# Kernel tuning notes

Measured on AMD Instinct MI355X. Metric: run time of the kernel, lower is better.

## Reference

```python
import jax, jax.numpy as jnp
import numpy as np

N = 40960      # nodes, level 0
E = 327680     # edges, level 0
N1 = 20480     # nodes after first graclus pool
E2 = 163840    # edges after first pool
N2 = 10240     # nodes after second graclus pool
B = 512        # graphs in batch
NCLS = 10


def seg_mean(v, idx, n):
    s = jax.ops.segment_sum(v, idx, num_segments=n)
    c = jax.ops.segment_sum(jnp.ones((idx.shape[0], 1), v.dtype), idx, num_segments=n)
    return s / jnp.maximum(c, 1.0)


def seg_max_f(v, idx, n):
    m = jax.ops.segment_max(v, idx, num_segments=n)
    return jnp.where(jnp.isneginf(m), 0.0, m)  # empty clusters -> 0


def cartesian(pos, ei):
    # PyG T.Cartesian(): cart = pos[row]-pos[col], normalized to [0,1]
    cart = pos[ei[0]] - pos[ei[1]]
    m = jnp.max(jnp.abs(cart))
    return cart / (2.0 * m) + 0.5


def nnconv_mean(x, ei, eattr, w1, b1, w2, b2, root, bias, n_nodes):
    # edge MLP -> per-edge weight matrix [E, Fin, Fout]
    fin, fout = root.shape
    h = jax.nn.relu(eattr @ w1 + b1) @ w2 + b2
    W = h.reshape(-1, fin, fout)
    src, dst = ei[0], ei[1]
    msg = jnp.einsum('ei,eio->eo', x[src], W)          # gather + per-edge matmul
    aggr = seg_mean(msg, dst, n_nodes)                 # scatter-mean
    return x @ root + aggr + bias


def setup_inputs() -> dict:
    key = jax.random.key(0)
    ks = jax.random.split(key, 24)
    inp = {}
    inp['x'] = jax.random.normal(ks[0], (N, 1), jnp.float32)
    inp['pos'] = jax.random.uniform(ks[1], (N, 2), jnp.float32) * 28.0
    inp['edge_attr'] = jax.random.uniform(ks[2], (E, 2), jnp.float32)
    inp['edge_index'] = jax.random.randint(ks[3], (2, E), 0, N)
    inp['batch'] = jnp.sort(jax.random.randint(ks[4], (N,), 0, B))
    inp['cluster1'] = jax.random.randint(ks[5], (N,), 0, N1)
    inp['edge_index2'] = jax.random.randint(ks[6], (2, E2), 0, N1)
    inp['cluster2'] = jax.random.randint(ks[7], (N1,), 0, N2)
    s = 0.1
    inp['nn1_w1'] = jax.random.normal(ks[8], (2, 25), jnp.float32) * s
    inp['nn1_b1'] = jnp.zeros((25,), jnp.float32)
    inp['nn1_w2'] = jax.random.normal(ks[9], (25, 32), jnp.float32) * s
    inp['nn1_b2'] = jnp.zeros((32,), jnp.float32)
    inp['root1'] = jax.random.normal(ks[10], (1, 32), jnp.float32) * s
    inp['bias1'] = jnp.zeros((32,), jnp.float32)
    inp['nn2_w1'] = jax.random.normal(ks[11], (2, 25), jnp.float32) * s
    inp['nn2_b1'] = jnp.zeros((25,), jnp.float32)
    inp['nn2_w2'] = jax.random.normal(ks[12], (25, 2048), jnp.float32) * s
    inp['nn2_b2'] = jnp.zeros((2048,), jnp.float32)
    inp['root2'] = jax.random.normal(ks[13], (32, 64), jnp.float32) * s
    inp['bias2'] = jnp.zeros((64,), jnp.float32)
    inp['fc1_w'] = jax.random.normal(ks[14], (64, 128), jnp.float32) * s
    inp['fc1_b'] = jnp.zeros((128,), jnp.float32)
    inp['fc2_w'] = jax.random.normal(ks[15], (128, NCLS), jnp.float32) * s
    inp['fc2_b'] = jnp.zeros((NCLS,), jnp.float32)
    return inp


def reference(x, pos, edge_attr, edge_index, batch, cluster1, edge_index2, cluster2,
              nn1_w1, nn1_b1, nn1_w2, nn1_b2, root1, bias1,
              nn2_w1, nn2_b1, nn2_w2, nn2_b2, root2, bias2,
              fc1_w, fc1_b, fc2_w, fc2_b):
    # conv1 + ELU
    x1 = jax.nn.elu(nnconv_mean(x, edge_index, edge_attr,
                                nn1_w1, nn1_b1, nn1_w2, nn1_b2, root1, bias1, N))
    # graclus max_pool (clusters precomputed): max features, mean pos, pooled batch
    x1p = seg_max_f(x1, cluster1, N1)
    pos1 = seg_mean(pos, cluster1, N1)
    batch1 = jnp.clip(jax.ops.segment_max(batch, cluster1, num_segments=N1), 0, B - 1)
    eattr2 = cartesian(pos1, edge_index2)  # transform=Cartesian on pooled graph
    # conv2 + ELU
    x2 = jax.nn.elu(nnconv_mean(x1p, edge_index2, eattr2,
                                nn2_w1, nn2_b1, nn2_w2, nn2_b2, root2, bias2, N1))
    # max_pool_x then global_mean_pool
    x2p = seg_max_f(x2, cluster2, N2)
    batch2 = jnp.clip(jax.ops.segment_max(batch1, cluster2, num_segments=N2), 0, B - 1)
    xg = seg_mean(x2p, batch2, B)
    h = jax.nn.elu(xg @ fc1_w + fc1_b)
    # dropout is identity in eval mode
    logits = h @ fc2_w + fc2_b
    return jax.nn.log_softmax(logits, axis=1)
```

## Files before the change

### kernel.cpp

```cpp
#include <hip/hip_runtime.h>
#include <hip/hip_bf16.h>
#include <limits.h>

#define NN   40960
#define EE   327680
#define NN1  20480
#define EE2  163840
#define NN2  10240
#define BB   512
#define NCLS 10

#define SEG1 160
#define SEG2 240
#define SEG3 320
#define SEG4 400
#define SBT  440

#define GEMM_BLKS 2080
#define R2_BLKS   640
#define CART_BLKS 640
#define PREP_BLKS 208

typedef short bf16x8 __attribute__((ext_vector_type(8)));
typedef float f32x4 __attribute__((ext_vector_type(4)));

__device__ __forceinline__ float elu_f(float v) { return v > 0.f ? v : (expf(v) - 1.f); }
__device__ __forceinline__ unsigned f2bf_bits(float v) {
    unsigned u = __float_as_uint(v);
    return (u + 0x7FFFu + ((u >> 16) & 1u)) >> 16;
}

__global__ void init_all(int* zbase, int zcount) {
    int i = blockIdx.x * 256 + threadIdx.x;
    if (i < zcount) zbase[i] = 0;
}

__global__ void deg_count(const int* __restrict__ ei, const int* __restrict__ ei2,
                          const int* __restrict__ cluster1, const int* __restrict__ cluster2,
                          int* deg1, int* degS, int* degD, int* degC1, int* degC2,
                          int* slot1, int* slotS, int* slotD, int* slotC1, int* slotC2) {
    int i = blockIdx.x * 256 + threadIdx.x;
    if (i < EE) slot1[i] = atomicAdd(deg1 + ei[EE + i], 1);
    if (i < EE2) {
        slotS[i] = atomicAdd(degS + ei2[i], 1);
        slotD[i] = atomicAdd(degD + ei2[EE2 + i], 1);
    }
    if (i < NN) slotC1[i] = atomicAdd(degC1 + cluster1[i], 1);
    if (i < NN1) slotC2[i] = atomicAdd(degC2 + cluster2[i], 1);
}

__global__ __launch_bounds__(256) void scan_partial(
    const int* __restrict__ deg1, const int* __restrict__ degS,
    const int* __restrict__ degD, const int* __restrict__ degC1,
    const int* __restrict__ degC2, int* __restrict__ part) {
    int b = blockIdx.x, t = threadIdx.x;
    const int* src;
    int off;
    if (b < SEG1)      { src = deg1;  off = b * 256; }
    else if (b < SEG2) { src = degS;  off = (b - SEG1) * 256; }
    else if (b < SEG3) { src = degD;  off = (b - SEG2) * 256; }
    else if (b < SEG4) { src = degC1; off = (b - SEG3) * 256; }
    else               { src = degC2; off = (b - SEG4) * 256; }
    int v = src[off + t];
#pragma unroll
    for (int o = 32; o; o >>= 1) v += __shfl_down(v, o, 64);
    __shared__ int sred[4];
    if ((t & 63) == 0) sred[t >> 6] = v;
    __syncthreads();
    if (t == 0) part[b] = sred[0] + sred[1] + sred[2] + sred[3];
}

__global__ __launch_bounds__(256) void scan_apply(
    const int* __restrict__ deg1, const int* __restrict__ degS,
    const int* __restrict__ degD, const int* __restrict__ degC1,
    const int* __restrict__ degC2, const int* __restrict__ part,
    int* rowptr1, int* rowptrS, int* rowptrD, int* rowptrC1, int* rowptrC2) {
    int b = blockIdx.x, t = threadIdx.x;
    const int* src;
    int* rp;
    int off, segLo;
    if (b < SEG1)      { src = deg1;  rp = rowptr1;  off = b * 256;          segLo = 0; }
    else if (b < SEG2) { src = degS;  rp = rowptrS;  off = (b - SEG1) * 256; segLo = SEG1; }
    else if (b < SEG3) { src = degD;  rp = rowptrD;  off = (b - SEG2) * 256; segLo = SEG2; }
    else if (b < SEG4) { src = degC1; rp = rowptrC1; off = (b - SEG3) * 256; segLo = SEG3; }
    else               { src = degC2; rp = rowptrC2; off = (b - SEG4) * 256; segLo = SEG4; }
    int bs = 0;
    for (int p = segLo + t; p < b; p += 256) bs += part[p];
#pragma unroll
    for (int o = 32; o; o >>= 1) bs += __shfl_down(bs, o, 64);
    __shared__ int sred[4];
    __shared__ int sh[256];
    if ((t & 63) == 0) sred[t >> 6] = bs;
    int v = src[off + t];
    sh[t] = v;
    __syncthreads();
    int base = sred[0] + sred[1] + sred[2] + sred[3];
#pragma unroll
    for (int o = 1; o < 256; o <<= 1) {
        int u = (t >= o) ? sh[t - o] : 0;
        __syncthreads();
        sh[t] += u;
        __syncthreads();
    }
    rp[off + t] = sh[t] - v + base;
    if (b == 0 && t == 0) {
        rowptr1[NN] = EE;
        rowptrS[NN1] = EE2;
        rowptrD[NN1] = EE2;
        rowptrC1[NN1] = NN;
        rowptrC2[NN2] = NN1;
    }
}

__global__ void fill_csr(const float* __restrict__ x, const float* __restrict__ ea,
                         const int* __restrict__ ei, const int* __restrict__ ei2,
                         const int* __restrict__ cluster1, const int* __restrict__ cluster2,
                         const int* __restrict__ rowptr1, const int* __restrict__ rowptrS,
                         const int* __restrict__ rowptrD, const int* __restrict__ rowptrC1,
                         const int* __restrict__ rowptrC2,
                         const int* __restrict__ slot1, const int* __restrict__ slotS,
                         const int* __restrict__ slotD, const int* __restrict__ slotC1,
                         const int* __restrict__ slotC2,
                         float4* __restrict__ eadj1, int4* __restrict__ cscRec,
                         int* __restrict__ memC1, int* __restrict__ memC2) {
    int i = blockIdx.x * 256 + threadIdx.x;
    if (i < EE) {
        int s = ei[i], d = ei[EE + i];
        eadj1[rowptr1[d] + slot1[i]] = make_float4(x[s], ea[2 * i], ea[2 * i + 1], 0.f);
    }
    if (i < EE2) {
        int s2 = ei2[i], d2 = ei2[EE2 + i];
        int q = rowptrS[s2] + slotS[i];
        int p2 = rowptrD[d2] + slotD[i];
        cscRec[q] = make_int4(s2, d2, p2, 0);
    }
    if (i < NN) memC1[rowptrC1[cluster1[i]] + slotC1[i]] = i;
    if (i < NN1) memC2[rowptrC2[cluster2[i]] + slotC2[i]] = i;
}

__global__ __launch_bounds__(256) void conv1_gather(
    const float* __restrict__ x, const int* __restrict__ rowptr1,
    const float4* __restrict__ eadj1,
    const float* __restrict__ w1, const float* __restrict__ b1,
    const float* __restrict__ w2, const float* __restrict__ b2,
    const float* __restrict__ root1, const float* __restrict__ bias1,
    float* __restrict__ x1) {
    int t = threadIdx.x;
    int j = t & 31;
    int n = blockIdx.x * 8 + (t >> 5);
    float w1x = 0.f, w1y = 0.f, b1j = 0.f;
    if (j < 25) { w1x = w1[j]; w1y = w1[25 + j]; b1j = b1[j]; }
    int r0 = rowptr1[n], r1 = rowptr1[n + 1];
    float agg = 0.f, sumx = 0.f;
    float4 e0 = make_float4(0.f, 0.f, 0.f, 0.f), e1 = e0;
    if (r0 < r1) e0 = eadj1[r0];
    if (r0 + 1 < r1) e1 = eadj1[r0 + 1];
    for (int p = r0; p < r1; p++) {
        float4 ed = e0;
        e0 = e1;
        if (p + 2 < r1) e1 = eadj1[p + 2];
        float h = fmaxf(fmaf(ed.y, w1x, fmaf(ed.z, w1y, b1j)), 0.f);
        agg = fmaf(ed.x, h, agg);
        sumx += ed.x;
    }
    float w2c[25];
#pragma unroll
    for (int k = 0; k < 25; k++) w2c[k] = w2[k * 32 + j];
    float m = sumx * b2[j];
#pragma unroll
    for (int k = 0; k < 25; k++) m = fmaf(__shfl(agg, k, 32), w2c[k], m);
    float deg = fmaxf((float)(r1 - r0), 1.f);
    float v = fmaf(x[n], root1[j], m / deg + bias1[j]);
    x1[(size_t)n * 32 + j] = elu_f(v);
}

__global__ __launch_bounds__(256) void pool1_gather(
    const float* __restrict__ x1, const float* __restrict__ pos,
    const int* __restrict__ batch, const int* __restrict__ rowptrC1,
    const int* __restrict__ memC1,
    float* __restrict__ x1p, unsigned short* __restrict__ x1pb,
    float* __restrict__ pos1, int* __restrict__ batch1) {
    int t = threadIdx.x;
    int j = t & 31;
    int c = blockIdx.x * 8 + (t >> 5);
    int r0 = rowptrC1[c], r1 = rowptrC1[c + 1];
    float mx = -INFINITY, sx = 0.f, sy = 0.f;
    int bmax = INT_MIN;
    for (int p = r0; p < r1; p++) {
        int v = memC1[p];
        mx = fmaxf(mx, x1[(size_t)v * 32 + j]);
        bmax = max(bmax, batch[v]);
        if (j == 0) {
            float2 pv = ((const float2*)pos)[v];
            sx += pv.x; sy += pv.y;
        }
    }
    float outv = (r0 < r1) ? mx : 0.f;
    x1p[(size_t)c * 32 + j] = outv;
    x1pb[(size_t)c * 32 + j] = (unsigned short)f2bf_bits(outv);
    if (j == 0) {
        float cn = fmaxf((float)(r1 - r0), 1.f);
        pos1[2 * c] = sx / cn;
        pos1[2 * c + 1] = sy / cn;
        batch1[c] = min(max(bmax, 0), BB - 1);
    }
}

__global__ void cartmax_prep(const float* __restrict__ pos1, const int* __restrict__ ei2,
                             unsigned* mBits,
                             const float* __restrict__ w2, const float* __restrict__ b2,
                             unsigned short* __restrict__ WextB) {
    int b = blockIdx.x;
    int t = threadIdx.x;
    if (b < CART_BLKS) {
        int e = b * 256 + t;
        float m = 0.f;
        if (e < EE2) {
            int r = ei2[e], c = ei2[EE2 + e];
            m = fmaxf(fabsf(pos1[2 * r] - pos1[2 * c]),
                      fabsf(pos1[2 * r + 1] - pos1[2 * c + 1]));
        }
        for (int off = 32; off; off >>= 1) m = fmaxf(m, __shfl_xor(m, off, 64));
        if ((t & 63) == 0) atomicMax(mBits, __float_as_uint(m));
    } else {
        int idx = (b - CART_BLKS) * 256 + t;
        if (idx >= 13 * 8 * 64 * 8) return;
        int j = idx & 7;
        int lane = (idx >> 3) & 63;
        int tile = (idx >> 9) & 7;
        int ky = idx >> 12;
        int h = tile >> 2, tt = tile & 3;
        int kmlp = 2 * ky + h;
        int o = tt * 16 + (lane & 15);
        int i = (lane >> 4) * 8 + j;
        float v = (kmlp < 25) ? w2[(size_t)kmlp * 2048 + i * 64 + o] : b2[i * 64 + o];
        WextB[idx] = (unsigned short)f2bf_bits(v);
    }
}

__global__ __launch_bounds__(256) void gemm_r2(
    const unsigned short* __restrict__ x1pb, const unsigned short* __restrict__ WextB,
    unsigned* __restrict__ Au,
    const int4* __restrict__ cscRec, const float* __restrict__ pos1,
    const float* __restrict__ w1, const float* __restrict__ b1,
    const unsigned* __restrict__ mBits, uint4* __restrict__ r2q) {
    int blk = blockIdx.x;
    int t = threadIdx.x;
    if (blk < GEMM_BLKS) {
        int lane = t & 63;
        int w = t >> 6;
        int bx = blk % 160;
        int ky = blk / 160;
        int m0 = bx * 128 + w * 32;
        int lo16 = lane & 15, hi4 = lane >> 4;
        bf16x8 bf[8];
        const bf16x8* Bp = (const bf16x8*)(WextB + (size_t)ky * 4096);
#pragma unroll
        for (int i = 0; i < 8; i++) bf[i] = Bp[i * 64 + lane];
        const f32x4 zero = {0.f, 0.f, 0.f, 0.f};
#pragma unroll
        for (int mt = 0; mt < 2; mt++) {
            int mbase = m0 + mt * 16;
            bf16x8 af = *(const bf16x8*)(x1pb + ((size_t)(mbase + lo16) * 32 + hi4 * 8));
            f32x4 acc[8];
#pragma unroll
            for (int i = 0; i < 8; i++)
                acc[i] = __builtin_amdgcn_mfma_f32_16x16x32_bf16(af, bf[i], zero, 0, 0, 0);
#pragma unroll
            for (int tt = 0; tt < 4; tt++) {
#pragma unroll
                for (int j = 0; j < 4; j++) {
                    int n = mbase + hi4 * 4 + j;
                    unsigned lo = f2bf_bits(acc[tt][j]);
                    unsigned hi = f2bf_bits(acc[4 + tt][j]);
                    Au[(size_t)n * 832 + ky * 64 + tt * 16 + lo16] = lo | (hi << 16);
                }
            }
        }
    } else {
        int q = (blk - GEMM_BLKS) * 256 + t;
        if (q >= EE2) return;
        int4 rec = cscRec[q];
        int s = rec.x, d = rec.y;
        float inv = 0.5f / __uint_as_float(*mBits);
        float2 ps = ((const float2*)pos1)[s];
        float2 pd = ((const float2*)pos1)[d];
        float cx = fmaf(ps.x - pd.x, inv, 0.5f);
        float cy = fmaf(ps.y - pd.y, inv, 0.5f);
        unsigned out[16];
#pragma unroll
        for (int ky = 0; ky < 13; ky++) {
            int k0 = 2 * ky, k1 = 2 * ky + 1;
            float rlo = fmaxf(fmaf(cx, w1[k0], fmaf(cy, w1[25 + k0], b1[k0])), 0.f);
            float rhi = 1.f;
            if (k1 < 25) rhi = fmaxf(fmaf(cx, w1[k1], fmaf(cy, w1[25 + k1], b1[k1])), 0.f);
            out[ky] = f2bf_bits(rlo) | (f2bf_bits(rhi) << 16);
        }
        out[13] = (unsigned)rec.z;
        out[14] = 0u; out[15] = 0u;
        uint4* dst = r2q + (size_t)q * 4;
        dst[0] = make_uint4(out[0], out[1], out[2], out[3]);
        dst[1] = make_uint4(out[4], out[5], out[6], out[7]);
        dst[2] = make_uint4(out[8], out[9], out[10], out[11]);
        dst[3] = make_uint4(out[12], out[13], out[14], out[15]);
    }
}

__global__ __launch_bounds__(256) void conv2_msg(
    const unsigned* __restrict__ Au, const uint4* __restrict__ r2q,
    const int* __restrict__ rowptrS, unsigned short* __restrict__ msgbuf) {
    int t = threadIdx.x;
    int lane = t & 63;
    int s = __builtin_amdgcn_readfirstlane(blockIdx.x * 4 + (t >> 6));
    unsigned au[13];
    const unsigned* Ab = Au + (size_t)s * 832 + lane;
#pragma unroll
    for (int ky = 0; ky < 13; ky++) au[ky] = Ab[ky * 64];
    int r0 = rowptrS[s], r1 = rowptrS[s + 1];
    uint4 A0, B0, C0, D0;
    if (r0 < r1) {
        const uint4* p4 = r2q + (size_t)r0 * 4;
        A0 = p4[0]; B0 = p4[1]; C0 = p4[2]; D0 = p4[3];
    }
    for (int q = r0; q < r1; q++) {
        uint4 a = A0, b = B0, c = C0, dd = D0;
        if (q + 1 < r1) {
            const uint4* p4 = r2q + (size_t)(q + 1) * 4;
            A0 = p4[0]; B0 = p4[1]; C0 = p4[2]; D0 = p4[3];
        }
        unsigned rr[13] = {a.x, a.y, a.z, a.w, b.x, b.y, b.z, b.w, c.x, c.y, c.z, c.w, dd.x};
        unsigned dstSlot = dd.y;
        float m0 = 0.f, m1 = 0.f;
#pragma unroll
        for (int ky = 0; ky < 13; ky++) {
            unsigned rp = rr[ky];
            unsigned ua = au[ky];
            m0 = fmaf(__uint_as_float(rp << 16), __uint_as_float(ua << 16), m0);
            m1 = fmaf(__uint_as_float(rp & 0xFFFF0000u), __uint_as_float(ua & 0xFFFF0000u), m1);
        }
        msgbuf[(size_t)dstSlot * 64 + lane] = (unsigned short)f2bf_bits(m0 + m1);
    }
}

__global__ __launch_bounds__(256) void conv2_fin(
    const unsigned short* __restrict__ msgbuf, const int* __restrict__ rowptrD,
    const float* __restrict__ x1p, const float* __restrict__ root2,
    const float* __restrict__ bias2, float* __restrict__ x2) {
    int t = threadIdx.x;
    int lane = t & 63;
    int n = blockIdx.x * 4 + (t >> 6);
    float Rr[32];
#pragma unroll
    for (int i = 0; i < 32; i++) Rr[i] = root2[i * 64 + lane];
    int r0 = rowptrD[n], r1 = rowptrD[n + 1];
    float acc = 0.f;
    for (int p = r0; p < r1; p++)
        acc += __uint_as_float((unsigned)msgbuf[(size_t)p * 64 + lane] << 16);
    float deg = fmaxf((float)(r1 - r0), 1.f);
    float xv = x1p[(size_t)n * 32 + (lane & 31)];
    float ra2 = bias2[lane];
#pragma unroll
    for (int i = 0; i < 32; i++) ra2 = fmaf(__shfl(xv, i, 64), Rr[i], ra2);
    x2[(size_t)n * 64 + lane] = elu_f(ra2 + acc / deg);
}

__global__ __launch_bounds__(256) void pool2_gather(
    const float* __restrict__ x2, const int* __restrict__ rowptrC2,
    const int* __restrict__ memC2, const int* __restrict__ batch1,
    float* __restrict__ xgsumS, float* __restrict__ gcntS) {
    int t = threadIdx.x;
    int lane = t & 63;
    int n2 = blockIdx.x * 4 + (t >> 6);
    int r0 = rowptrC2[n2], r1 = rowptrC2[n2 + 1];
    float mx = -INFINITY;
    int bmax = INT_MIN;
    for (int p = r0; p < r1; p++) {
        int m = memC2[p];
        mx = fmaxf(mx, x2[(size_t)m * 64 + lane]);
        bmax = max(bmax, batch1[m]);
    }
    float v = (r0 < r1) ? mx : 0.f;
    int b = min(max(bmax, 0), BB - 1);
    int shard = n2 & 7;
    atomicAdd(xgsumS + ((size_t)shard * BB + b) * 64 + lane, v);
    if (lane == 0) atomicAdd(gcntS + shard * BB + b, 1.f);
}

__global__ __launch_bounds__(128) void head_kernel(
    const float* __restrict__ xgsumS, const float* __restrict__ gcntS,
    const float* __restrict__ fc1w, const float* __restrict__ fc1b,
    const float* __restrict__ fc2w, const float* __restrict__ fc2b,
    float* __restrict__ out) {
    int b = blockIdx.x;
    int t = threadIdx.x;
    __shared__ float xg[64];
    __shared__ float h[128];
    __shared__ float lg[NCLS];
    __shared__ float red[2];
    __shared__ float cntsh;
    float s = 0.f;
    if (t < 64) {
#pragma unroll
        for (int sh = 0; sh < 8; sh++) s += xgsumS[((size_t)sh * BB + b) * 64 + t];
    }
    if (t == 64) {
        float c = 0.f;
#pragma unroll
        for (int sh = 0; sh < 8; sh++) c += gcntS[sh * BB + b];
        cntsh = fmaxf(c, 1.f);
    }
    __syncthreads();
    if (t < 64) xg[t] = s / cntsh;
    __syncthreads();
    float a1 = fc1b[t];
    for (int i = 0; i < 64; i++) a1 = fmaf(xg[i], fc1w[i * 128 + t], a1);
    h[t] = elu_f(a1);
    __syncthreads();
    if (t < NCLS) {
        float a = fc2b[t];
        for (int j = 0; j < 128; j++) a = fmaf(h[j], fc2w[j * NCLS + t], a);
        lg[t] = a;
    }
    __syncthreads();
    if (t == 0) {
        float mx = lg[0];
        for (int i = 1; i < NCLS; i++) mx = fmaxf(mx, lg[i]);
        float se = 0.f;
        for (int i = 0; i < NCLS; i++) se += expf(lg[i] - mx);
        red[0] = mx;
        red[1] = logf(se);
    }
    __syncthreads();
    if (t < NCLS) out[(size_t)b * NCLS + t] = lg[t] - red[0] - red[1];
}

extern "C" void kernel_launch(void* const* d_in, const int* in_sizes, int n_in,
                              void* d_out, int out_size, void* d_ws, size_t ws_size,
                              hipStream_t stream) {
    const float* x = (const float*)d_in[0];
    const float* pos = (const float*)d_in[1];
    const float* edge_attr = (const float*)d_in[2];
    const int* ei = (const int*)d_in[3];
    const int* batch = (const int*)d_in[4];
    const int* cluster1 = (const int*)d_in[5];
    const int* ei2 = (const int*)d_in[6];
    const int* cluster2 = (const int*)d_in[7];
    const float* nn1_w1 = (const float*)d_in[8];
    const float* nn1_b1 = (const float*)d_in[9];
    const float* nn1_w2 = (const float*)d_in[10];
    const float* nn1_b2 = (const float*)d_in[11];
    const float* root1 = (const float*)d_in[12];
    const float* bias1 = (const float*)d_in[13];
    const float* nn2_w1 = (const float*)d_in[14];
    const float* nn2_b1 = (const float*)d_in[15];
    const float* nn2_w2 = (const float*)d_in[16];
    const float* nn2_b2 = (const float*)d_in[17];
    const float* root2 = (const float*)d_in[18];
    const float* bias2 = (const float*)d_in[19];
    const float* fc1w = (const float*)d_in[20];
    const float* fc1b = (const float*)d_in[21];
    const float* fc2w = (const float*)d_in[22];
    const float* fc2b = (const float*)d_in[23];

    float* ws = (float*)d_ws;
    constexpr size_t OFF_DEG1 = 0;
    constexpr size_t OFF_DEGS = OFF_DEG1 + NN;
    constexpr size_t OFF_DEGD = OFF_DEGS + NN1;
    constexpr size_t OFF_DEGC1 = OFF_DEGD + NN1;
    constexpr size_t OFF_DEGC2 = OFF_DEGC1 + NN1;
    constexpr size_t OFF_XGS = OFF_DEGC2 + NN2;
    constexpr size_t OFF_GCS = OFF_XGS + (size_t)8 * BB * 64;
    constexpr size_t OFF_MBITS = OFF_GCS + 8 * BB;
    constexpr size_t ZTOT = OFF_MBITS + 4;
    constexpr size_t OFF_PART = ZTOT;
    constexpr size_t OFF_ROWPTR1 = OFF_PART + SBT;
    constexpr size_t OFF_ROWPTRS = OFF_ROWPTR1 + NN + 4;
    constexpr size_t OFF_ROWPTRD = OFF_ROWPTRS + NN1 + 4;
    constexpr size_t OFF_ROWPTRC1 = OFF_ROWPTRD + NN1 + 4;
    constexpr size_t OFF_ROWPTRC2 = OFF_ROWPTRC1 + NN1 + 4;
    constexpr size_t OFF_SLOT1 = OFF_ROWPTRC2 + NN2 + 4;
    constexpr size_t OFF_SLOTS = OFF_SLOT1 + EE;
    constexpr size_t OFF_SLOTD = OFF_SLOTS + EE2;
    constexpr size_t OFF_SLOTC1 = OFF_SLOTD + EE2;
    constexpr size_t OFF_SLOTC2 = OFF_SLOTC1 + NN;
    constexpr size_t OFF_CSCREC = OFF_SLOTC2 + NN1;
    constexpr size_t OFF_MEMC1 = OFF_CSCREC + (size_t)EE2 * 4;
    constexpr size_t OFF_MEMC2 = OFF_MEMC1 + NN;
    constexpr size_t OFF_X1 = OFF_MEMC2 + NN1;
    constexpr size_t OFF_X1P = OFF_X1 + (size_t)NN * 32;
    constexpr size_t OFF_X1PB = OFF_X1P + (size_t)NN1 * 32;
    constexpr size_t OFF_POS1 = OFF_X1PB + (size_t)NN1 * 16;
    constexpr size_t OFF_BATCH1 = OFF_POS1 + (size_t)NN1 * 2;
    constexpr size_t OFF_X2 = OFF_BATCH1 + NN1;
    constexpr size_t OFF_WEXTB = OFF_X2 + (size_t)NN1 * 64;
    constexpr size_t OFF_UA = OFF_WEXTB + 26624;
    constexpr size_t UASZ = (size_t)EE2 * 16;
    constexpr size_t OFF_MSG = OFF_UA + UASZ;
    constexpr size_t OFF_AU = OFF_MSG + (size_t)EE2 * 32;

    int* deg1 = (int*)(ws + OFF_DEG1);
    int* degS = (int*)(ws + OFF_DEGS);
    int* degD = (int*)(ws + OFF_DEGD);
    int* degC1 = (int*)(ws + OFF_DEGC1);
    int* degC2 = (int*)(ws + OFF_DEGC2);
    float* xgsumS = ws + OFF_XGS;
    float* gcntS = ws + OFF_GCS;
    unsigned* mBits = (unsigned*)(ws + OFF_MBITS);
    int* part = (int*)(ws + OFF_PART);
    int* rowptr1 = (int*)(ws + OFF_ROWPTR1);
    int* rowptrS = (int*)(ws + OFF_ROWPTRS);
    int* rowptrD = (int*)(ws + OFF_ROWPTRD);
    int* rowptrC1 = (int*)(ws + OFF_ROWPTRC1);
    int* rowptrC2 = (int*)(ws + OFF_ROWPTRC2);
    int* slot1 = (int*)(ws + OFF_SLOT1);
    int* slotS = (int*)(ws + OFF_SLOTS);
    int* slotD = (int*)(ws + OFF_SLOTD);
    int* slotC1 = (int*)(ws + OFF_SLOTC1);
    int* slotC2 = (int*)(ws + OFF_SLOTC2);
    int4* cscRec = (int4*)(ws + OFF_CSCREC);
    int* memC1 = (int*)(ws + OFF_MEMC1);
    int* memC2 = (int*)(ws + OFF_MEMC2);
    float* x1 = ws + OFF_X1;
    float* x1p = ws + OFF_X1P;
    unsigned short* x1pb = (unsigned short*)(ws + OFF_X1PB);
    float* pos1 = ws + OFF_POS1;
    int* batch1 = (int*)(ws + OFF_BATCH1);
    float* x2 = ws + OFF_X2;
    unsigned short* WextB = (unsigned short*)(ws + OFF_WEXTB);
    float4* eadj1 = (float4*)(ws + OFF_UA);
    uint4* r2q = (uint4*)(ws + OFF_UA);
    unsigned short* msgbuf = (unsigned short*)(ws + OFF_MSG);
    unsigned* Au = (unsigned*)(ws + OFF_AU);

    init_all<<<(int)((ZTOT + 255) / 256), 256, 0, stream>>>((int*)d_ws, (int)ZTOT);
    deg_count<<<EE / 256, 256, 0, stream>>>(ei, ei2, cluster1, cluster2,
                                            deg1, degS, degD, degC1, degC2,
                                            slot1, slotS, slotD, slotC1, slotC2);
    scan_partial<<<SBT, 256, 0, stream>>>(deg1, degS, degD, degC1, degC2, part);
    scan_apply<<<SBT, 256, 0, stream>>>(deg1, degS, degD, degC1, degC2, part,
                                        rowptr1, rowptrS, rowptrD, rowptrC1, rowptrC2);
    fill_csr<<<EE / 256, 256, 0, stream>>>(x, edge_attr, ei, ei2, cluster1, cluster2,
                                           rowptr1, rowptrS, rowptrD, rowptrC1, rowptrC2,
                                           slot1, slotS, slotD, slotC1, slotC2,
                                           eadj1, cscRec, memC1, memC2);
    conv1_gather<<<NN / 8, 256, 0, stream>>>(x, rowptr1, eadj1,
                                             nn1_w1, nn1_b1, nn1_w2, nn1_b2, root1, bias1, x1);
    pool1_gather<<<NN1 / 8, 256, 0, stream>>>(x1, pos, batch, rowptrC1, memC1,
                                              x1p, x1pb, pos1, batch1);
    cartmax_prep<<<CART_BLKS + PREP_BLKS, 256, 0, stream>>>(pos1, ei2, mBits,
                                                            nn2_w2, nn2_b2, WextB);
    gemm_r2<<<GEMM_BLKS + R2_BLKS, 256, 0, stream>>>(x1pb, WextB, Au,
                                                     cscRec, pos1, nn2_w1, nn2_b1,
                                                     mBits, r2q);
    conv2_msg<<<NN1 / 4, 256, 0, stream>>>(Au, r2q, rowptrS, msgbuf);
    conv2_fin<<<NN1 / 4, 256, 0, stream>>>(msgbuf, rowptrD, x1p, root2, bias2, x2);
    pool2_gather<<<NN2 / 4, 256, 0, stream>>>(x2, rowptrC2, memC2, batch1, xgsumS, gcntS);
    head_kernel<<<BB, 128, 0, stream>>>(xgsumS, gcntS, fc1w, fc1b, fc2w, fc2b,
                                        (float*)d_out);
}
```

Measured before the change: 200.5 us.

## Fuse per-node MFMA projection into conv2 message kernel via shared memory

The MFMA GEMM that projects pooled node features onto the edge-MLP weight basis now runs inside the conv2 message kernel, one 16-node tile per block. The products stay in LDS instead of being written to and re-read from a global Au buffer of 832 words per node. The r2 edge-feature computation moves to its own kernel. This removes global traffic for the intermediate, but recomputes the WextB loads per block, serialises the GEMM and gather phases behind a barrier, and uses about 53KB of LDS per block, which limits occupancy.

```diff
diff --git a/kernel.cpp b/kernel.cpp
--- a/kernel.cpp
+++ b/kernel.cpp
@@ -16,8 +16,6 @@
 #define SEG4 400
 #define SBT  440
 
-#define GEMM_BLKS 2080
-#define R2_BLKS   640
 #define CART_BLKS 640
 #define PREP_BLKS 208
 
@@ -238,107 +236,98 @@
     }
 }
 
-__global__ __launch_bounds__(256) void gemm_r2(
-    const unsigned short* __restrict__ x1pb, const unsigned short* __restrict__ WextB,
-    unsigned* __restrict__ Au,
+__global__ __launch_bounds__(256) void r2_kernel(
     const int4* __restrict__ cscRec, const float* __restrict__ pos1,
     const float* __restrict__ w1, const float* __restrict__ b1,
     const unsigned* __restrict__ mBits, uint4* __restrict__ r2q) {
-    int blk = blockIdx.x;
-    int t = threadIdx.x;
-    if (blk < GEMM_BLKS) {
-        int lane = t & 63;
-        int w = t >> 6;
-        int bx = blk % 160;
-        int ky = blk / 160;
-        int m0 = bx * 128 + w * 32;
-        int lo16 = lane & 15, hi4 = lane >> 4;
-        bf16x8 bf[8];
+    int q = blockIdx.x * 256 + threadIdx.x;
+    if (q >= EE2) return;
+    int4 rec = cscRec[q];
+    int s = rec.x, d = rec.y;
+    float inv = 0.5f / __uint_as_float(*mBits);
+    float2 ps = ((const float2*)pos1)[s];
+    float2 pd = ((const float2*)pos1)[d];
+    float cx = fmaf(ps.x - pd.x, inv, 0.5f);
+    float cy = fmaf(ps.y - pd.y, inv, 0.5f);
+    unsigned out[16];
+#pragma unroll
+    for (int ky = 0; ky < 13; ky++) {
+        int k0 = 2 * ky, k1 = 2 * ky + 1;
+        float rlo = fmaxf(fmaf(cx, w1[k0], fmaf(cy, w1[25 + k0], b1[k0])), 0.f);
+        float rhi = 1.f;
+        if (k1 < 25) rhi = fmaxf(fmaf(cx, w1[k1], fmaf(cy, w1[25 + k1], b1[k1])), 0.f);
+        out[ky] = f2bf_bits(rlo) | (f2bf_bits(rhi) << 16);
+    }
+    out[13] = (unsigned)rec.z;
+    out[14] = 0u; out[15] = 0u;
+    uint4* dst = r2q + (size_t)q * 4;
+    dst[0] = make_uint4(out[0], out[1], out[2], out[3]);
+    dst[1] = make_uint4(out[4], out[5], out[6], out[7]);
+    dst[2] = make_uint4(out[8], out[9], out[10], out[11]);
+    dst[3] = make_uint4(out[12], out[13], out[14], out[15]);
+}
+
+__global__ __launch_bounds__(256) void conv2_fused(
+    const unsigned short* __restrict__ x1pb, const unsigned short* __restrict__ WextB,
+    const uint4* __restrict__ r2q, const int* __restrict__ rowptrS,
+    unsigned short* __restrict__ msgbuf) {
+    __shared__ unsigned lau[16 * 833];
+    int t = threadIdx.x;
+    int lane = t & 63;
+    int w = t >> 6;
+    int s0 = blockIdx.x * 16;
+    int lo16 = lane & 15, hi4 = lane >> 4;
+    bf16x8 af = *(const bf16x8*)(x1pb + ((size_t)(s0 + lo16) * 32 + hi4 * 8));
+    const f32x4 zero = {0.f, 0.f, 0.f, 0.f};
+    for (int ky = w; ky < 13; ky += 4) {
         const bf16x8* Bp = (const bf16x8*)(WextB + (size_t)ky * 4096);
-#pragma unroll
-        for (int i = 0; i < 8; i++) bf[i] = Bp[i * 64 + lane];
-        const f32x4 zero = {0.f, 0.f, 0.f, 0.f};
-#pragma unroll
-        for (int mt = 0; mt < 2; mt++) {
-            int mbase = m0 + mt * 16;
-            bf16x8 af = *(const bf16x8*)(x1pb + ((size_t)(mbase + lo16) * 32 + hi4 * 8));
-            f32x4 acc[8];
-#pragma unroll
-            for (int i = 0; i < 8; i++)
-                acc[i] = __builtin_amdgcn_mfma_f32_16x16x32_bf16(af, bf[i], zero, 0, 0, 0);
-#pragma unroll
-            for (int tt = 0; tt < 4; tt++) {
-#pragma unroll
-                for (int j = 0; j < 4; j++) {
-                    int n = mbase + hi4 * 4 + j;
-                    unsigned lo = f2bf_bits(acc[tt][j]);
-                    unsigned hi = f2bf_bits(acc[4 + tt][j]);
-                    Au[(size_t)n * 832 + ky * 64 + tt * 16 + lo16] = lo | (hi << 16);
-                }
+        f32x4 acc[8];
+#pragma unroll
+        for (int i = 0; i < 8; i++) {
+            bf16x8 bf = Bp[i * 64 + lane];
+            acc[i] = __builtin_amdgcn_mfma_f32_16x16x32_bf16(af, bf, zero, 0, 0, 0);
+        }
+#pragma unroll
+        for (int tt = 0; tt < 4; tt++) {
+#pragma unroll
+            for (int j = 0; j < 4; j++) {
+                int row = hi4 * 4 + j;
+                unsigned lo = f2bf_bits(acc[tt][j]);
+                unsigned hi = f2bf_bits(acc[4 + tt][j]);
+                lau[row * 833 + ky * 64 + tt * 16 + lo16] = lo | (hi << 16);
             }
         }
-    } else {
-        int q = (blk - GEMM_BLKS) * 256 + t;
-        if (q >= EE2) return;
-        int4 rec = cscRec[q];
-        int s = rec.x, d = rec.y;
-        float inv = 0.5f / __uint_as_float(*mBits);
-        float2 ps = ((const float2*)pos1)[s];
-        float2 pd = ((const float2*)pos1)[d];
-        float cx = fmaf(ps.x - pd.x, inv, 0.5f);
-        float cy = fmaf(ps.y - pd.y, inv, 0.5f);
-        unsigned out[16];
-#pragma unroll
-        for (int ky = 0; ky < 13; ky++) {
-            int k0 = 2 * ky, k1 = 2 * ky + 1;
-            float rlo = fmaxf(fmaf(cx, w1[k0], fmaf(cy, w1[25 + k0], b1[k0])), 0.f);
-            float rhi = 1.f;
-            if (k1 < 25) rhi = fmaxf(fmaf(cx, w1[k1], fmaf(cy, w1[25 + k1], b1[k1])), 0.f);
-            out[ky] = f2bf_bits(rlo) | (f2bf_bits(rhi) << 16);
-        }
-        out[13] = (unsigned)rec.z;
-        out[14] = 0u; out[15] = 0u;
-        uint4* dst = r2q + (size_t)q * 4;
-        dst[0] = make_uint4(out[0], out[1], out[2], out[3]);
-        dst[1] = make_uint4(out[4], out[5], out[6], out[7]);
-        dst[2] = make_uint4(out[8], out[9], out[10], out[11]);
-        dst[3] = make_uint4(out[12], out[13], out[14], out[15]);
-    }
-}
-
-__global__ __launch_bounds__(256) void conv2_msg(
-    const unsigned* __restrict__ Au, const uint4* __restrict__ r2q,
-    const int* __restrict__ rowptrS, unsigned short* __restrict__ msgbuf) {
-    int t = threadIdx.x;
-    int lane = t & 63;
-    int s = __builtin_amdgcn_readfirstlane(blockIdx.x * 4 + (t >> 6));
-    unsigned au[13];
-    const unsigned* Ab = Au + (size_t)s * 832 + lane;
-#pragma unroll
-    for (int ky = 0; ky < 13; ky++) au[ky] = Ab[ky * 64];
-    int r0 = rowptrS[s], r1 = rowptrS[s + 1];
-    uint4 A0, B0, C0, D0;
-    if (r0 < r1) {
-        const uint4* p4 = r2q + (size_t)r0 * 4;
-        A0 = p4[0]; B0 = p4[1]; C0 = p4[2]; D0 = p4[3];
-    }
-    for (int q = r0; q < r1; q++) {
-        uint4 a = A0, b = B0, c = C0, dd = D0;
-        if (q + 1 < r1) {
-            const uint4* p4 = r2q + (size_t)(q + 1) * 4;
+    }
+    __syncthreads();
+    for (int si = 0; si < 4; si++) {
+        int sl = w * 4 + si;
+        int s = s0 + sl;
+        int r0 = rowptrS[s], r1 = rowptrS[s + 1];
+        const unsigned* la = lau + sl * 833;
+        uint4 A0, B0, C0, D0;
+        if (r0 < r1) {
+            const uint4* p4 = r2q + (size_t)r0 * 4;
             A0 = p4[0]; B0 = p4[1]; C0 = p4[2]; D0 = p4[3];
         }
-        unsigned rr[13] = {a.x, a.y, a.z, a.w, b.x, b.y, b.z, b.w, c.x, c.y, c.z, c.w, dd.x};
-        unsigned dstSlot = dd.y;
-        float m0 = 0.f, m1 = 0.f;
-#pragma unroll
-        for (int ky = 0; ky < 13; ky++) {
-            unsigned rp = rr[ky];
-            unsigned ua = au[ky];
-            m0 = fmaf(__uint_as_float(rp << 16), __uint_as_float(ua << 16), m0);
-            m1 = fmaf(__uint_as_float(rp & 0xFFFF0000u), __uint_as_float(ua & 0xFFFF0000u), m1);
+        for (int q = r0; q < r1; q++) {
+            uint4 a = A0, b = B0, c = C0, dd = D0;
+            if (q + 1 < r1) {
+                const uint4* p4 = r2q + (size_t)(q + 1) * 4;
+                A0 = p4[0]; B0 = p4[1]; C0 = p4[2]; D0 = p4[3];
+            }
+            unsigned rr[13] = {a.x, a.y, a.z, a.w, b.x, b.y, b.z, b.w,
+                               c.x, c.y, c.z, c.w, dd.x};
+            unsigned dstSlot = dd.y;
+            float m0 = 0.f, m1 = 0.f;
+#pragma unroll
+            for (int ky = 0; ky < 13; ky++) {
+                unsigned rp = rr[ky];
+                unsigned ua = la[ky * 64 + lane];
+                m0 = fmaf(__uint_as_float(rp << 16), __uint_as_float(ua << 16), m0);
+                m1 = fmaf(__uint_as_float(rp & 0xFFFF0000u), __uint_as_float(ua & 0xFFFF0000u), m1);
+            }
+            msgbuf[(size_t)dstSlot * 64 + lane] = (unsigned short)f2bf_bits(m0 + m1);
         }
-        msgbuf[(size_t)dstSlot * 64 + lane] = (unsigned short)f2bf_bits(m0 + m1);
     }
 }
 
@@ -496,7 +485,6 @@
     constexpr size_t OFF_UA = OFF_WEXTB + 26624;
     constexpr size_t UASZ = (size_t)EE2 * 16;
     constexpr size_t OFF_MSG = OFF_UA + UASZ;
-    constexpr size_t OFF_AU = OFF_MSG + (size_t)EE2 * 32;
 
     int* deg1 = (int*)(ws + OFF_DEG1);
     int* degS = (int*)(ws + OFF_DEGS);
@@ -530,7 +518,6 @@
     float4* eadj1 = (float4*)(ws + OFF_UA);
     uint4* r2q = (uint4*)(ws + OFF_UA);
     unsigned short* msgbuf = (unsigned short*)(ws + OFF_MSG);
-    unsigned* Au = (unsigned*)(ws + OFF_AU);
 
     init_all<<<(int)((ZTOT + 255) / 256), 256, 0, stream>>>((int*)d_ws, (int)ZTOT);
     deg_count<<<EE / 256, 256, 0, stream>>>(ei, ei2, cluster1, cluster2,
@@ -549,10 +536,8 @@
                                               x1p, x1pb, pos1, batch1);
     cartmax_prep<<<CART_BLKS + PREP_BLKS, 256, 0, stream>>>(pos1, ei2, mBits,
                                                             nn2_w2, nn2_b2, WextB);
-    gemm_r2<<<GEMM_BLKS + R2_BLKS, 256, 0, stream>>>(x1pb, WextB, Au,
-                                                     cscRec, pos1, nn2_w1, nn2_b1,
-                                                     mBits, r2q);
-    conv2_msg<<<NN1 / 4, 256, 0, stream>>>(Au, r2q, rowptrS, msgbuf);
+    r2_kernel<<<EE2 / 256, 256, 0, stream>>>(cscRec, pos1, nn2_w1, nn2_b1, mBits, r2q);
+    conv2_fused<<<NN1 / 16, 256, 0, stream>>>(x1pb, WextB, r2q, rowptrS, msgbuf);
     conv2_fin<<<NN1 / 4, 256, 0, stream>>>(msgbuf, rowptrD, x1p, root2, bias2, x2);
     pool2_gather<<<NN2 / 4, 256, 0, stream>>>(x2, rowptrC2, memC2, batch1, xgsumS, gcntS);
     head_kernel<<<BB, 128, 0, stream>>>(xgsumS, gcntS, fc1w, fc1b, fc2w, fc2b,
```

After: 211.9 us. 5.7% more time.
